# Performance work log

Hardware: AMD Instinct MI355X
Metric: run time of the kernel (lower is better)

The kernel has to match this reference:

```python
import jax, jax.numpy as jnp
import numpy as np

D_MODEL = 1024
NUM_HEADS = 16
D_K = D_MODEL // NUM_HEADS
D_FF = 4096
EPS = 1e-5


def _layernorm(x, gamma, beta):
    mu = jnp.mean(x, axis=-1, keepdims=True)
    var = jnp.mean(jnp.square(x - mu), axis=-1, keepdims=True)
    return (x - mu) * jax.lax.rsqrt(var + EPS) * gamma + beta


def setup_inputs() -> dict:
    key = jax.random.key(0)
    ks = jax.random.split(key, 16)
    B, S = 4, 2048
    s_in = 1.0 / np.sqrt(D_MODEL)
    s_ff = 1.0 / np.sqrt(D_FF)
    inp = {
        "x": jax.random.normal(ks[0], (B, S, D_MODEL), jnp.float32),
        "src_mask": jnp.ones((B, 1, 1, S), jnp.int32),
        "w_q": jax.random.normal(ks[1], (D_MODEL, D_MODEL), jnp.float32) * s_in,
        "b_q": jnp.zeros((D_MODEL,), jnp.float32),
        "w_k": jax.random.normal(ks[2], (D_MODEL, D_MODEL), jnp.float32) * s_in,
        "b_k": jnp.zeros((D_MODEL,), jnp.float32),
        "w_v": jax.random.normal(ks[3], (D_MODEL, D_MODEL), jnp.float32) * s_in,
        "b_v": jnp.zeros((D_MODEL,), jnp.float32),
        "w_o": jax.random.normal(ks[4], (D_MODEL, D_MODEL), jnp.float32) * s_in,
        "b_o": jnp.zeros((D_MODEL,), jnp.float32),
        "w1": jax.random.normal(ks[5], (D_MODEL, D_FF), jnp.float32) * s_in,
        "b1": jnp.zeros((D_FF,), jnp.float32),
        "w2": jax.random.normal(ks[6], (D_FF, D_MODEL), jnp.float32) * s_ff,
        "b2": jnp.zeros((D_MODEL,), jnp.float32),
        "g1": jnp.ones((D_MODEL,), jnp.float32),
        "be1": jnp.zeros((D_MODEL,), jnp.float32),
        "g2": jnp.ones((D_MODEL,), jnp.float32),
        "be2": jnp.zeros((D_MODEL,), jnp.float32),
    }
    return inp


def reference(x, src_mask, w_q, b_q, w_k, b_k, w_v, b_v, w_o, b_o,
              w1, b1, w2, b2, g1, be1, g2, be2):
    B, S, _ = x.shape

    def split_heads(t):  # [B,S,D] -> [B,H,S,dk]
        return t.reshape(B, S, NUM_HEADS, D_K).transpose(0, 2, 1, 3)

    q = split_heads(x @ w_q + b_q)
    k = split_heads(x @ w_k + b_k)
    v = split_heads(x @ w_v + b_v)

    scores = jnp.einsum("bhqd,bhkd->bhqk", q, k) / np.sqrt(D_K)
    scores = jnp.where(src_mask == 0, -jnp.inf, scores)
    attn = jax.nn.softmax(scores, axis=-1)
    ctx = jnp.einsum("bhqk,bhkd->bhqd", attn, v)
    merged = ctx.transpose(0, 2, 1, 3).reshape(B, S, D_MODEL)
    attn_out = merged @ w_o + b_o

    h = _layernorm(x + attn_out, g1, be1)
    ff = jax.nn.relu(h @ w1 + b1) @ w2 + b2
    return _layernorm(h + ff, g2, be2)
```

## Files before the change

### kernel.cpp

```cpp
#include <hip/hip_runtime.h>

typedef unsigned short u16;
typedef __attribute__((ext_vector_type(4))) unsigned short u16x4;
typedef __attribute__((ext_vector_type(8))) short bf16x8;
typedef __attribute__((ext_vector_type(4))) float f32x4;

__device__ inline float bf2f(u16 u) {
  union { unsigned int i; float f; } v; v.i = ((unsigned int)u) << 16; return v.f;
}
__device__ inline u16 f2bf(float f) {
  union { float f; unsigned int i; } v; v.f = f;
  unsigned int r = v.i + 0x7fffu + ((v.i >> 16) & 1u);
  return (u16)(r >> 16);
}

typedef const __attribute__((address_space(1))) unsigned int* gas_t;
typedef __attribute__((address_space(3))) unsigned int* las_t;
__device__ inline void gload_lds16(const u16* g, u16* l) {
  __builtin_amdgcn_global_load_lds((gas_t)(unsigned long long)(const void*)g,
                                   (las_t)(unsigned int)(unsigned long long)(void*)l,
                                   16, 0, 0);
}

__global__ __launch_bounds__(256) void cvt_bf16(const float* __restrict__ src,
                                                u16* __restrict__ dst, int n) {
  int i = (blockIdx.x * 256 + threadIdx.x) * 4;
  if (i >= n) return;
  float4 v = *(const float4*)(src + i);
  u16x4 o;
  o.x = f2bf(v.x); o.y = f2bf(v.y); o.z = f2bf(v.z); o.w = f2bf(v.w);
  *(u16x4*)(dst + i) = o;
}

__global__ __launch_bounds__(256) void transpose_f32_bf16(const float* __restrict__ src,
                                                          u16* __restrict__ dst,
                                                          int R, int C) {
  __shared__ u16 tile[32][33];
  int tx = threadIdx.x & 31, ty = threadIdx.x >> 5;
  int c0 = blockIdx.x * 32, r0 = blockIdx.y * 32;
  #pragma unroll
  for (int i = ty; i < 32; i += 8)
    tile[i][tx] = f2bf(src[(size_t)(r0 + i) * C + c0 + tx]);
  __syncthreads();
  #pragma unroll
  for (int i = ty; i < 32; i += 8)
    dst[(size_t)(c0 + i) * R + r0 + tx] = tile[tx][i];
}

__global__ __launch_bounds__(256) void transpose_v(const u16* __restrict__ Vb,
                                                   u16* __restrict__ VT,
                                                   int B, int S, int H) {
  const int D = H * 64;
  __shared__ u16 tile[32][33];
  int tx = threadIdx.x & 31, ty = threadIdx.x >> 5;
  int s0 = blockIdx.x * 32, d0 = blockIdx.y * 32;
  int bh = blockIdx.z;
  int b = bh / H, h = bh % H;
  #pragma unroll
  for (int i = ty; i < 32; i += 8)
    tile[i][tx] = Vb[(size_t)(b * S + s0 + i) * D + h * 64 + d0 + tx];
  __syncthreads();
  #pragma unroll
  for (int i = ty; i < 32; i += 8)
    VT[((size_t)bh * 64 + d0 + i) * S + s0 + tx] = tile[tx][i];
}

__global__ __launch_bounds__(256) void gemm_bt(const u16* __restrict__ A,
                                               const u16* __restrict__ Bt,
                                               const float* __restrict__ bias,
                                               u16* __restrict__ C,
                                               int M, int N, int K, int relu) {
  __shared__ u16 As[128 * 32];
  __shared__ u16 Bs[128 * 32];
  const int tid = threadIdx.x;
  const int lane = tid & 63, wid = tid >> 6;
  const int lr = lane & 15, quad = lane >> 4;
  const int wm = (wid >> 1) * 64, wn = (wid & 1) * 64;
  const int m0 = blockIdx.y * 128, n0 = blockIdx.x * 128;
  const int lrow = lane >> 2;
  const int lcol = (lane & 3) * 8;

  f32x4 acc[4][4];
  const f32x4 zero = {0.f, 0.f, 0.f, 0.f};
  #pragma unroll
  for (int mt = 0; mt < 4; ++mt)
    #pragma unroll
    for (int nt = 0; nt < 4; ++nt) acc[mt][nt] = zero;

  for (int k0 = 0; k0 < K; k0 += 32) {
    #pragma unroll
    for (int it = 0; it < 2; ++it) {
      int rbase = wid * 32 + it * 16;
      gload_lds16(A + (size_t)(m0 + rbase + lrow) * K + k0 + lcol, &As[rbase * 32]);
      gload_lds16(Bt + (size_t)(n0 + rbase + lrow) * K + k0 + lcol, &Bs[rbase * 32]);
    }
    __syncthreads();
    bf16x8 af[4], bfr[4];
    #pragma unroll
    for (int mt = 0; mt < 4; ++mt)
      af[mt] = *(const bf16x8*)(&As[(wm + mt * 16 + lr) * 32 + quad * 8]);
    #pragma unroll
    for (int nt = 0; nt < 4; ++nt)
      bfr[nt] = *(const bf16x8*)(&Bs[(wn + nt * 16 + lr) * 32 + quad * 8]);
    #pragma unroll
    for (int mt = 0; mt < 4; ++mt)
      #pragma unroll
      for (int nt = 0; nt < 4; ++nt)
        acc[mt][nt] = __builtin_amdgcn_mfma_f32_16x16x32_bf16(af[mt], bfr[nt], acc[mt][nt], 0, 0, 0);
    __syncthreads();
  }

  #pragma unroll
  for (int nt = 0; nt < 4; ++nt) {
    int n = n0 + wn + nt * 16 + lr;
    float bv = bias[n];
    #pragma unroll
    for (int mt = 0; mt < 4; ++mt) {
      #pragma unroll
      for (int i = 0; i < 4; ++i) {
        int m = m0 + wm + mt * 16 + quad * 4 + i;
        float v = acc[mt][nt][i] + bv;
        if (relu) v = fmaxf(v, 0.f);
        C[(size_t)m * N + n] = f2bf(v);
      }
    }
  }
}

__global__ __launch_bounds__(256) void flash_attn(const u16* __restrict__ Q,
                                                  const u16* __restrict__ Kg,
                                                  const u16* __restrict__ VT,
                                                  const int* __restrict__ mask,
                                                  u16* __restrict__ ctx,
                                                  int B, int S, int H) {
  const int D = H * 64;
  __shared__ u16 kt_lds[64 * 72];
  __shared__ u16 vt_lds[64 * 72];
  __shared__ u16 p_lds[4 * 16 * 72];
  const int tid = threadIdx.x;
  const int lane = tid & 63, wid = tid >> 6;
  const int lr = lane & 15, quad = lane >> 4;
  const int bh = blockIdx.y;
  const int b = bh / H, h = bh % H;
  const int q0 = blockIdx.x * 64;
  const u16* vt_base = VT + (size_t)bh * 64 * S;

  bf16x8 qf[2];
  {
    int qm = q0 + wid * 16 + lr;
    const u16* qptr = Q + (size_t)(b * S + qm) * D + h * 64;
    qf[0] = *(const bf16x8*)(qptr + quad * 8);
    qf[1] = *(const bf16x8*)(qptr + 32 + quad * 8);
  }

  float m_i[4], l_i[4], O[4][4];
  #pragma unroll
  for (int i = 0; i < 4; ++i) {
    m_i[i] = -1e30f; l_i[i] = 0.f;
    #pragma unroll
    for (int nt = 0; nt < 4; ++nt) O[nt][i] = 0.f;
  }

  for (int kt = 0; kt < S; kt += 64) {
    #pragma unroll
    for (int it = 0; it < 2; ++it) {
      int c = tid + it * 256;
      int r = c >> 3;
      int cc = (c & 7) * 8;
      uint4 kv = *(const uint4*)(Kg + (size_t)(b * S + kt + r) * D + h * 64 + cc);
      *(uint4*)(&kt_lds[r * 72 + cc]) = kv;
      uint4 vv = *(const uint4*)(vt_base + (size_t)r * S + kt + cc);
      *(uint4*)(&vt_lds[r * 72 + cc]) = vv;
    }
    __syncthreads();

    float s[4][4];
    #pragma unroll
    for (int st = 0; st < 4; ++st) {
      f32x4 c = {0.f, 0.f, 0.f, 0.f};
      #pragma unroll
      for (int ch = 0; ch < 2; ++ch) {
        bf16x8 bfrag = *(const bf16x8*)(&kt_lds[(st * 16 + lr) * 72 + ch * 32 + quad * 8]);
        c = __builtin_amdgcn_mfma_f32_16x16x32_bf16(qf[ch], bfrag, c, 0, 0, 0);
      }
      int kpos = kt + st * 16 + lr;
      float mb = mask[b * S + kpos] ? 0.f : -1e30f;
      #pragma unroll
      for (int i = 0; i < 4; ++i) s[st][i] = c[i] * 0.125f + mb;
    }

    float al[4];
    #pragma unroll
    for (int i = 0; i < 4; ++i) {
      float r = fmaxf(fmaxf(s[0][i], s[1][i]), fmaxf(s[2][i], s[3][i]));
      #pragma unroll
      for (int mm = 1; mm < 16; mm <<= 1) r = fmaxf(r, __shfl_xor(r, mm, 64));
      float mn = fmaxf(m_i[i], r);
      al[i] = __expf(m_i[i] - mn);
      m_i[i] = mn;
    }
    float rs[4] = {0.f, 0.f, 0.f, 0.f};
    #pragma unroll
    for (int st = 0; st < 4; ++st)
      #pragma unroll
      for (int i = 0; i < 4; ++i) {
        float p = __expf(s[st][i] - m_i[i]);
        s[st][i] = p; rs[i] += p;
      }
    #pragma unroll
    for (int i = 0; i < 4; ++i) {
      float r = rs[i];
      #pragma unroll
      for (int mm = 1; mm < 16; mm <<= 1) r += __shfl_xor(r, mm, 64);
      l_i[i] = l_i[i] * al[i] + r;
    }

    u16* pw = &p_lds[wid * 16 * 72];
    #pragma unroll
    for (int st = 0; st < 4; ++st)
      #pragma unroll
      for (int i = 0; i < 4; ++i)
        pw[(quad * 4 + i) * 72 + st * 16 + lr] = f2bf(s[st][i]);

    #pragma unroll
    for (int nt = 0; nt < 4; ++nt) {
      f32x4 c;
      c[0] = O[nt][0] * al[0]; c[1] = O[nt][1] * al[1];
      c[2] = O[nt][2] * al[2]; c[3] = O[nt][3] * al[3];
      #pragma unroll
      for (int ch = 0; ch < 2; ++ch) {
        bf16x8 af = *(const bf16x8*)(&pw[lr * 72 + ch * 32 + quad * 8]);
        bf16x8 bfv = *(const bf16x8*)(&vt_lds[(nt * 16 + lr) * 72 + ch * 32 + quad * 8]);
        c = __builtin_amdgcn_mfma_f32_16x16x32_bf16(af, bfv, c, 0, 0, 0);
      }
      O[nt][0] = c[0]; O[nt][1] = c[1]; O[nt][2] = c[2]; O[nt][3] = c[3];
    }
    __syncthreads();
  }

  #pragma unroll
  for (int i = 0; i < 4; ++i) {
    float inv = 1.f / fmaxf(l_i[i], 1e-30f);
    int q = q0 + wid * 16 + quad * 4 + i;
    u16* op = ctx + (size_t)(b * S + q) * D + h * 64;
    #pragma unroll
    for (int nt = 0; nt < 4; ++nt) op[nt * 16 + lr] = f2bf(O[nt][i] * inv);
  }
}

__device__ inline float block_reduce_sum(float v, float* sbuf) {
  #pragma unroll
  for (int m = 1; m < 64; m <<= 1) v += __shfl_xor(v, m, 64);
  int w = threadIdx.x >> 6;
  if ((threadIdx.x & 63) == 0) sbuf[w] = v;
  __syncthreads();
  v = sbuf[0] + sbuf[1] + sbuf[2] + sbuf[3];
  __syncthreads();
  return v;
}

__global__ __launch_bounds__(256) void add_ln(const float* __restrict__ a32,
                                              const u16* __restrict__ a16,
                                              const u16* __restrict__ b,
                                              const float* __restrict__ g,
                                              const float* __restrict__ be,
                                              u16* __restrict__ out16,
                                              float* __restrict__ out32, int D) {
  __shared__ float sbuf[4];
  int row = blockIdx.x;
  size_t base = (size_t)row * D;
  int i = threadIdx.x * 4;
  float v[4];
  {
    u16x4 bv = *(const u16x4*)(b + base + i);
    if (a32) {
      float4 av = *(const float4*)(a32 + base + i);
      v[0] = av.x + bf2f(bv.x); v[1] = av.y + bf2f(bv.y);
      v[2] = av.z + bf2f(bv.z); v[3] = av.w + bf2f(bv.w);
    } else {
      u16x4 av = *(const u16x4*)(a16 + base + i);
      v[0] = bf2f(av.x) + bf2f(bv.x); v[1] = bf2f(av.y) + bf2f(bv.y);
      v[2] = bf2f(av.z) + bf2f(bv.z); v[3] = bf2f(av.w) + bf2f(bv.w);
    }
  }
  float sum = v[0] + v[1] + v[2] + v[3];
  sum = block_reduce_sum(sum, sbuf);
  float mean = sum / (float)D;
  float var = 0.f;
  #pragma unroll
  for (int j = 0; j < 4; ++j) { float d = v[j] - mean; var += d * d; }
  var = block_reduce_sum(var, sbuf);
  float rstd = rsqrtf(var / (float)D + 1e-5f);
  float4 gv = *(const float4*)(g + i);
  float4 bev = *(const float4*)(be + i);
  float o0 = (v[0] - mean) * rstd * gv.x + bev.x;
  float o1 = (v[1] - mean) * rstd * gv.y + bev.y;
  float o2 = (v[2] - mean) * rstd * gv.z + bev.z;
  float o3 = (v[3] - mean) * rstd * gv.w + bev.w;
  if (out32) {
    float4 o = {o0, o1, o2, o3};
    *(float4*)(out32 + base + i) = o;
  } else {
    u16x4 o;
    o.x = f2bf(o0); o.y = f2bf(o1); o.z = f2bf(o2); o.w = f2bf(o3);
    *(u16x4*)(out16 + base + i) = o;
  }
}

extern "C" void kernel_launch(void* const* d_in, const int* in_sizes, int n_in,
                              void* d_out, int out_size, void* d_ws, size_t ws_size,
                              hipStream_t stream) {
  (void)in_sizes; (void)n_in; (void)out_size; (void)ws_size;
  const float* x   = (const float*)d_in[0];
  const int* mask  = (const int*)d_in[1];
  const float* wq  = (const float*)d_in[2];
  const float* bq  = (const float*)d_in[3];
  const float* wk  = (const float*)d_in[4];
  const float* bk  = (const float*)d_in[5];
  const float* wv  = (const float*)d_in[6];
  const float* bv  = (const float*)d_in[7];
  const float* wo  = (const float*)d_in[8];
  const float* bo  = (const float*)d_in[9];
  const float* w1  = (const float*)d_in[10];
  const float* b1  = (const float*)d_in[11];
  const float* w2  = (const float*)d_in[12];
  const float* b2  = (const float*)d_in[13];
  const float* g1  = (const float*)d_in[14];
  const float* be1 = (const float*)d_in[15];
  const float* g2  = (const float*)d_in[16];
  const float* be2 = (const float*)d_in[17];

  const int B = 4, S = 2048, D = 1024, H = 16, DFF = 4096;
  const size_t TOK = (size_t)B * S;
  const size_t TD = TOK * D;

  u16* ws  = (u16*)d_ws;
  u16* xb  = ws;
  u16* Qb  = ws + 1 * TD;
  u16* Kb  = ws + 2 * TD;
  u16* Vb  = ws + 3 * TD;
  u16* CTX = ws + 4 * TD;
  u16* ATT = ws + 5 * TD;
  u16* Hb  = ws + 6 * TD;
  u16* WQT = ws + 7 * TD;
  u16* WKT = WQT + (size_t)D * D;
  u16* WVT = WKT + (size_t)D * D;
  u16* WOT = WVT + (size_t)D * D;
  u16* W1T = WQT + 4 * (size_t)D * D;
  u16* VT  = xb;
  u16* FF1 = Qb;
  u16* FF2 = ATT;
  u16* W2T = WQT;

  dim3 blk(256);

  cvt_bf16<<<dim3((unsigned)(TD / (256 * 4))), blk, 0, stream>>>(x, xb, (int)TD);

  transpose_f32_bf16<<<dim3(D / 32, D / 32), blk, 0, stream>>>(wq, WQT, D, D);
  transpose_f32_bf16<<<dim3(D / 32, D / 32), blk, 0, stream>>>(wk, WKT, D, D);
  transpose_f32_bf16<<<dim3(D / 32, D / 32), blk, 0, stream>>>(wv, WVT, D, D);
  transpose_f32_bf16<<<dim3(D / 32, D / 32), blk, 0, stream>>>(wo, WOT, D, D);
  transpose_f32_bf16<<<dim3(DFF / 32, D / 32), blk, 0, stream>>>(w1, W1T, D, DFF);

  gemm_bt<<<dim3(D / 128, TOK / 128), blk, 0, stream>>>(xb, WQT, bq, Qb, (int)TOK, D, D, 0);
  gemm_bt<<<dim3(D / 128, TOK / 128), blk, 0, stream>>>(xb, WKT, bk, Kb, (int)TOK, D, D, 0);
  gemm_bt<<<dim3(D / 128, TOK / 128), blk, 0, stream>>>(xb, WVT, bv, Vb, (int)TOK, D, D, 0);

  transpose_v<<<dim3(S / 32, 2, B * H), blk, 0, stream>>>(Vb, VT, B, S, H);

  flash_attn<<<dim3(S / 64, B * H), blk, 0, stream>>>(Qb, Kb, VT, mask, CTX, B, S, H);

  gemm_bt<<<dim3(D / 128, TOK / 128), blk, 0, stream>>>(CTX, WOT, bo, ATT, (int)TOK, D, D, 0);

  transpose_f32_bf16<<<dim3(D / 32, DFF / 32), blk, 0, stream>>>(w2, W2T, DFF, D);

  add_ln<<<dim3((unsigned)TOK), blk, 0, stream>>>(x, (const u16*)nullptr, ATT, g1, be1,
                                                  Hb, (float*)nullptr, D);

  gemm_bt<<<dim3(DFF / 128, TOK / 128), blk, 0, stream>>>(Hb, W1T, b1, FF1, (int)TOK, DFF, D, 1);
  gemm_bt<<<dim3(D / 128, TOK / 128), blk, 0, stream>>>(FF1, W2T, b2, FF2, (int)TOK, D, DFF, 0);

  add_ln<<<dim3((unsigned)TOK), blk, 0, stream>>>((const float*)nullptr, Hb, FF2, g2, be2,
                                                  (u16*)nullptr, (float*)d_out, D);
}
```

Baseline: 754.2 us.

## Fuse QKV projections into one GEMM and transpose flash-attention MFMA layout

Concatenates the Q/K/V weights and biases so a single GEMM with N=3072 writes an interleaved QKV buffer, and flash attention and the V transpose now read from it with a stride. The aim is to cut kernel launches and improve GPU occupancy for the projection. Flash attention also swaps the MFMA operand order, so each lane owns one query row. Row max and sum then need only two cross-lane shuffles instead of per-row 16-lane reductions, and P and output stores become vectorized. Mask values are staged once per tile in LDS, which adds a small kernel and reuses CTX memory as the bias buffer.

```diff
diff --git a/kernel.cpp b/kernel.cpp
--- a/kernel.cpp
+++ b/kernel.cpp
@@ -32,6 +32,15 @@
   *(u16x4*)(dst + i) = o;
 }
 
+__global__ __launch_bounds__(256) void concat3(const float* __restrict__ a,
+                                               const float* __restrict__ b,
+                                               const float* __restrict__ c,
+                                               float* __restrict__ o, int n) {
+  int i = blockIdx.x * 256 + threadIdx.x;
+  if (i >= n) return;
+  o[i] = a[i]; o[n + i] = b[i]; o[2 * n + i] = c[i];
+}
+
 __global__ __launch_bounds__(256) void transpose_f32_bf16(const float* __restrict__ src,
                                                           u16* __restrict__ dst,
                                                           int R, int C) {
@@ -47,10 +56,9 @@
     dst[(size_t)(c0 + i) * R + r0 + tx] = tile[tx][i];
 }
 
-__global__ __launch_bounds__(256) void transpose_v(const u16* __restrict__ Vb,
+__global__ __launch_bounds__(256) void transpose_v(const u16* __restrict__ src,
                                                    u16* __restrict__ VT,
-                                                   int B, int S, int H) {
-  const int D = H * 64;
+                                                   int B, int S, int H, int RS, int CO) {
   __shared__ u16 tile[32][33];
   int tx = threadIdx.x & 31, ty = threadIdx.x >> 5;
   int s0 = blockIdx.x * 32, d0 = blockIdx.y * 32;
@@ -58,7 +66,7 @@
   int b = bh / H, h = bh % H;
   #pragma unroll
   for (int i = ty; i < 32; i += 8)
-    tile[i][tx] = Vb[(size_t)(b * S + s0 + i) * D + h * 64 + d0 + tx];
+    tile[i][tx] = src[(size_t)(b * S + s0 + i) * RS + CO + h * 64 + d0 + tx];
   __syncthreads();
   #pragma unroll
   for (int i = ty; i < 32; i += 8)
@@ -127,16 +135,16 @@
   }
 }
 
-__global__ __launch_bounds__(256) void flash_attn(const u16* __restrict__ Q,
-                                                  const u16* __restrict__ Kg,
+__global__ __launch_bounds__(256) void flash_attn(const u16* __restrict__ Qp,
+                                                  const u16* __restrict__ Kp,
                                                   const u16* __restrict__ VT,
                                                   const int* __restrict__ mask,
                                                   u16* __restrict__ ctx,
-                                                  int B, int S, int H) {
-  const int D = H * 64;
+                                                  int B, int S, int H, int QSTR) {
   __shared__ u16 kt_lds[64 * 72];
   __shared__ u16 vt_lds[64 * 72];
   __shared__ u16 p_lds[4 * 16 * 72];
+  __shared__ float msk_lds[64];
   const int tid = threadIdx.x;
   const int lane = tid & 63, wid = tid >> 6;
   const int lr = lane & 15, quad = lane >> 4;
@@ -148,18 +156,17 @@
   bf16x8 qf[2];
   {
     int qm = q0 + wid * 16 + lr;
-    const u16* qptr = Q + (size_t)(b * S + qm) * D + h * 64;
+    const u16* qptr = Qp + (size_t)(b * S + qm) * QSTR + h * 64;
     qf[0] = *(const bf16x8*)(qptr + quad * 8);
     qf[1] = *(const bf16x8*)(qptr + 32 + quad * 8);
   }
 
-  float m_i[4], l_i[4], O[4][4];
-  #pragma unroll
-  for (int i = 0; i < 4; ++i) {
-    m_i[i] = -1e30f; l_i[i] = 0.f;
-    #pragma unroll
-    for (int nt = 0; nt < 4; ++nt) O[nt][i] = 0.f;
-  }
+  float m_i = -1e30f, l_i = 0.f;
+  float O[4][4];
+  #pragma unroll
+  for (int nt = 0; nt < 4; ++nt)
+    #pragma unroll
+    for (int i = 0; i < 4; ++i) O[nt][i] = 0.f;
 
   for (int kt = 0; kt < S; kt += 64) {
     #pragma unroll
@@ -167,11 +174,12 @@
       int c = tid + it * 256;
       int r = c >> 3;
       int cc = (c & 7) * 8;
-      uint4 kv = *(const uint4*)(Kg + (size_t)(b * S + kt + r) * D + h * 64 + cc);
+      uint4 kv = *(const uint4*)(Kp + (size_t)(b * S + kt + r) * QSTR + h * 64 + cc);
       *(uint4*)(&kt_lds[r * 72 + cc]) = kv;
       uint4 vv = *(const uint4*)(vt_base + (size_t)r * S + kt + cc);
       *(uint4*)(&vt_lds[r * 72 + cc]) = vv;
     }
+    if (tid < 64) msk_lds[tid] = mask[b * S + kt + tid] ? 0.f : -1e30f;
     __syncthreads();
 
     float s[4][4];
@@ -180,71 +188,72 @@
       f32x4 c = {0.f, 0.f, 0.f, 0.f};
       #pragma unroll
       for (int ch = 0; ch < 2; ++ch) {
-        bf16x8 bfrag = *(const bf16x8*)(&kt_lds[(st * 16 + lr) * 72 + ch * 32 + quad * 8]);
-        c = __builtin_amdgcn_mfma_f32_16x16x32_bf16(qf[ch], bfrag, c, 0, 0, 0);
+        bf16x8 kf = *(const bf16x8*)(&kt_lds[(st * 16 + lr) * 72 + ch * 32 + quad * 8]);
+        c = __builtin_amdgcn_mfma_f32_16x16x32_bf16(kf, qf[ch], c, 0, 0, 0);
       }
-      int kpos = kt + st * 16 + lr;
-      float mb = mask[b * S + kpos] ? 0.f : -1e30f;
-      #pragma unroll
-      for (int i = 0; i < 4; ++i) s[st][i] = c[i] * 0.125f + mb;
-    }
-
-    float al[4];
-    #pragma unroll
-    for (int i = 0; i < 4; ++i) {
-      float r = fmaxf(fmaxf(s[0][i], s[1][i]), fmaxf(s[2][i], s[3][i]));
-      #pragma unroll
-      for (int mm = 1; mm < 16; mm <<= 1) r = fmaxf(r, __shfl_xor(r, mm, 64));
-      float mn = fmaxf(m_i[i], r);
-      al[i] = __expf(m_i[i] - mn);
-      m_i[i] = mn;
-    }
-    float rs[4] = {0.f, 0.f, 0.f, 0.f};
+      float4 mv = *(const float4*)(&msk_lds[st * 16 + quad * 4]);
+      s[st][0] = c[0] * 0.125f + mv.x;
+      s[st][1] = c[1] * 0.125f + mv.y;
+      s[st][2] = c[2] * 0.125f + mv.z;
+      s[st][3] = c[3] * 0.125f + mv.w;
+    }
+
+    float tmax = s[0][0];
     #pragma unroll
     for (int st = 0; st < 4; ++st)
       #pragma unroll
+      for (int i = 0; i < 4; ++i) tmax = fmaxf(tmax, s[st][i]);
+    tmax = fmaxf(tmax, __shfl_xor(tmax, 16, 64));
+    tmax = fmaxf(tmax, __shfl_xor(tmax, 32, 64));
+    float mn = fmaxf(m_i, tmax);
+    float al = __expf(m_i - mn);
+    m_i = mn;
+    float rs = 0.f;
+    #pragma unroll
+    for (int st = 0; st < 4; ++st)
+      #pragma unroll
       for (int i = 0; i < 4; ++i) {
-        float p = __expf(s[st][i] - m_i[i]);
-        s[st][i] = p; rs[i] += p;
+        float p = __expf(s[st][i] - mn);
+        s[st][i] = p; rs += p;
       }
-    #pragma unroll
-    for (int i = 0; i < 4; ++i) {
-      float r = rs[i];
-      #pragma unroll
-      for (int mm = 1; mm < 16; mm <<= 1) r += __shfl_xor(r, mm, 64);
-      l_i[i] = l_i[i] * al[i] + r;
-    }
+    rs += __shfl_xor(rs, 16, 64);
+    rs += __shfl_xor(rs, 32, 64);
+    l_i = l_i * al + rs;
 
     u16* pw = &p_lds[wid * 16 * 72];
     #pragma unroll
-    for (int st = 0; st < 4; ++st)
-      #pragma unroll
-      for (int i = 0; i < 4; ++i)
-        pw[(quad * 4 + i) * 72 + st * 16 + lr] = f2bf(s[st][i]);
+    for (int st = 0; st < 4; ++st) {
+      u16x4 pk;
+      pk.x = f2bf(s[st][0]); pk.y = f2bf(s[st][1]);
+      pk.z = f2bf(s[st][2]); pk.w = f2bf(s[st][3]);
+      *(u16x4*)(&pw[lr * 72 + st * 16 + quad * 4]) = pk;
+    }
 
     #pragma unroll
     for (int nt = 0; nt < 4; ++nt) {
       f32x4 c;
-      c[0] = O[nt][0] * al[0]; c[1] = O[nt][1] * al[1];
-      c[2] = O[nt][2] * al[2]; c[3] = O[nt][3] * al[3];
+      c[0] = O[nt][0] * al; c[1] = O[nt][1] * al;
+      c[2] = O[nt][2] * al; c[3] = O[nt][3] * al;
       #pragma unroll
       for (int ch = 0; ch < 2; ++ch) {
-        bf16x8 af = *(const bf16x8*)(&pw[lr * 72 + ch * 32 + quad * 8]);
-        bf16x8 bfv = *(const bf16x8*)(&vt_lds[(nt * 16 + lr) * 72 + ch * 32 + quad * 8]);
-        c = __builtin_amdgcn_mfma_f32_16x16x32_bf16(af, bfv, c, 0, 0, 0);
+        bf16x8 vf = *(const bf16x8*)(&vt_lds[(nt * 16 + lr) * 72 + ch * 32 + quad * 8]);
+        bf16x8 pf = *(const bf16x8*)(&pw[lr * 72 + ch * 32 + quad * 8]);
+        c = __builtin_amdgcn_mfma_f32_16x16x32_bf16(vf, pf, c, 0, 0, 0);
       }
       O[nt][0] = c[0]; O[nt][1] = c[1]; O[nt][2] = c[2]; O[nt][3] = c[3];
     }
     __syncthreads();
   }
 
-  #pragma unroll
-  for (int i = 0; i < 4; ++i) {
-    float inv = 1.f / fmaxf(l_i[i], 1e-30f);
-    int q = q0 + wid * 16 + quad * 4 + i;
-    u16* op = ctx + (size_t)(b * S + q) * D + h * 64;
-    #pragma unroll
-    for (int nt = 0; nt < 4; ++nt) op[nt * 16 + lr] = f2bf(O[nt][i] * inv);
+  float linv = 1.f / fmaxf(l_i, 1e-30f);
+  int q = q0 + wid * 16 + lr;
+  u16* op = ctx + (size_t)(b * S + q) * (H * 64) + h * 64;
+  #pragma unroll
+  for (int nt = 0; nt < 4; ++nt) {
+    u16x4 o;
+    o.x = f2bf(O[nt][0] * linv); o.y = f2bf(O[nt][1] * linv);
+    o.z = f2bf(O[nt][2] * linv); o.w = f2bf(O[nt][3] * linv);
+    *(u16x4*)(op + nt * 16 + quad * 4) = o;
   }
 }
 
@@ -331,44 +340,41 @@
   const float* be2 = (const float*)d_in[17];
 
   const int B = 4, S = 2048, D = 1024, H = 16, DFF = 4096;
+  const int D3 = 3 * D;
   const size_t TOK = (size_t)B * S;
   const size_t TD = TOK * D;
 
-  u16* ws  = (u16*)d_ws;
-  u16* xb  = ws;
-  u16* Qb  = ws + 1 * TD;
-  u16* Kb  = ws + 2 * TD;
-  u16* Vb  = ws + 3 * TD;
-  u16* CTX = ws + 4 * TD;
-  u16* ATT = ws + 5 * TD;
-  u16* Hb  = ws + 6 * TD;
-  u16* WQT = ws + 7 * TD;
-  u16* WKT = WQT + (size_t)D * D;
-  u16* WVT = WKT + (size_t)D * D;
-  u16* WOT = WVT + (size_t)D * D;
-  u16* W1T = WQT + 4 * (size_t)D * D;
-  u16* VT  = xb;
-  u16* FF1 = Qb;
-  u16* FF2 = ATT;
-  u16* W2T = WQT;
+  u16* ws   = (u16*)d_ws;
+  u16* QKVp = ws;
+  u16* xb   = ws + 3 * TD;
+  u16* VT   = xb;
+  u16* CTX  = ws + 4 * TD;
+  u16* ATT  = ws + 5 * TD;
+  u16* Hb   = ws + 6 * TD;
+  u16* QKVT = ws + 7 * TD;
+  u16* WOT  = QKVT + 3 * (size_t)D * D;
+  u16* W1T  = WOT + (size_t)D * D;
+  u16* FF1  = ws;
+  u16* FF2  = ATT;
+  u16* W2T  = QKVT;
+  float* biasc = (float*)CTX;
 
   dim3 blk(256);
 
   cvt_bf16<<<dim3((unsigned)(TD / (256 * 4))), blk, 0, stream>>>(x, xb, (int)TD);
-
-  transpose_f32_bf16<<<dim3(D / 32, D / 32), blk, 0, stream>>>(wq, WQT, D, D);
-  transpose_f32_bf16<<<dim3(D / 32, D / 32), blk, 0, stream>>>(wk, WKT, D, D);
-  transpose_f32_bf16<<<dim3(D / 32, D / 32), blk, 0, stream>>>(wv, WVT, D, D);
+  concat3<<<dim3(4), blk, 0, stream>>>(bq, bk, bv, biasc, D);
+
+  transpose_f32_bf16<<<dim3(D / 32, D / 32), blk, 0, stream>>>(wq, QKVT, D, D);
+  transpose_f32_bf16<<<dim3(D / 32, D / 32), blk, 0, stream>>>(wk, QKVT + (size_t)D * D, D, D);
+  transpose_f32_bf16<<<dim3(D / 32, D / 32), blk, 0, stream>>>(wv, QKVT + 2 * (size_t)D * D, D, D);
   transpose_f32_bf16<<<dim3(D / 32, D / 32), blk, 0, stream>>>(wo, WOT, D, D);
   transpose_f32_bf16<<<dim3(DFF / 32, D / 32), blk, 0, stream>>>(w1, W1T, D, DFF);
 
-  gemm_bt<<<dim3(D / 128, TOK / 128), blk, 0, stream>>>(xb, WQT, bq, Qb, (int)TOK, D, D, 0);
-  gemm_bt<<<dim3(D / 128, TOK / 128), blk, 0, stream>>>(xb, WKT, bk, Kb, (int)TOK, D, D, 0);
-  gemm_bt<<<dim3(D / 128, TOK / 128), blk, 0, stream>>>(xb, WVT, bv, Vb, (int)TOK, D, D, 0);
-
-  transpose_v<<<dim3(S / 32, 2, B * H), blk, 0, stream>>>(Vb, VT, B, S, H);
-
-  flash_attn<<<dim3(S / 64, B * H), blk, 0, stream>>>(Qb, Kb, VT, mask, CTX, B, S, H);
+  gemm_bt<<<dim3(D3 / 128, TOK / 128), blk, 0, stream>>>(xb, QKVT, biasc, QKVp, (int)TOK, D3, D, 0);
+
+  transpose_v<<<dim3(S / 32, 2, B * H), blk, 0, stream>>>(QKVp, VT, B, S, H, D3, 2 * D);
+
+  flash_attn<<<dim3(S / 64, B * H), blk, 0, stream>>>(QKVp, QKVp + D, VT, mask, CTX, B, S, H, D3);
 
   gemm_bt<<<dim3(D / 128, TOK / 128), blk, 0, stream>>>(CTX, WOT, bo, ATT, (int)TOK, D, D, 0);
 
```

Result: faster. 669.4 us (-11.2%).
